# Optimization experiments

Hardware: AMD Instinct MI355X
Metric: run time of the kernel (lower is better)

Reference implementation:

```python
import jax, jax.numpy as jnp
import numpy as np

B, T, H = 16, 512, 1024
L, D = 8192, 256

def setup_inputs() -> dict:
    key = jax.random.key(0)
    k1, k2, k3, k4, k5 = jax.random.split(key, 5)
    X = jax.random.normal(k1, (B, T, H), dtype=jnp.float32)
    attention_mask = jnp.ones((B, T), dtype=jnp.int32)
    queries = jax.random.normal(k2, (L, D), dtype=jnp.float32) * 0.02
    Wk = jax.random.normal(k3, (D, H), dtype=jnp.float32) * (1.0 / np.sqrt(H))
    Wv = jax.random.normal(k4, (D, H), dtype=jnp.float32) * (1.0 / np.sqrt(H))
    out_weight = jax.random.normal(k5, (L, D), dtype=jnp.float32) * 0.02
    out_bias = jnp.zeros((L,), dtype=jnp.float32)
    return {"X": X, "attention_mask": attention_mask, "queries": queries,
            "Wk": Wk, "Wv": Wv, "out_weight": out_weight, "out_bias": out_bias}

def reference(X, attention_mask, queries, Wk, Wv, out_weight, out_bias):
    # K, V: [B, T, D] (nn.Linear with weight [D, H], no bias)
    K = jnp.einsum('bth,dh->btd', X, Wk)
    V = jnp.einsum('bth,dh->btd', X, Wv)
    scale = 1.0 / jnp.sqrt(jnp.asarray(K.shape[-1], dtype=K.dtype))
    # attention logits: [B, L, T]
    attn_logits = jnp.einsum('ld,btd->blt', queries, K) * scale
    neg = jnp.finfo(attn_logits.dtype).min
    attn_logits = jnp.where(attention_mask[:, None, :] == 0, neg, attn_logits)
    attn = jax.nn.softmax(attn_logits, axis=-1)
    # per-label context: [B, L, D]
    ctx = jnp.einsum('blt,btd->bld', attn, V)
    # fused per-label output projection: [B, L]
    logits = jnp.einsum('bld,ld->bl', ctx, out_weight) + out_bias[None, :]
    return logits
```

## Files before the change

kernel.cpp:

```cpp
#include <hip/hip_runtime.h>
#include <hip/hip_bf16.h>


typedef __bf16 bf16x8 __attribute__((ext_vector_type(8)));
typedef float f32x4 __attribute__((ext_vector_type(4)));

__device__ __forceinline__ unsigned short f2bf(float f) {
    unsigned int u = __builtin_bit_cast(unsigned int, f);
    unsigned int lsb = (u >> 16) & 1u;
    u += 0x7fffu + lsb;
    return (unsigned short)(u >> 16);
}

__device__ __forceinline__ void gld_lds16(const void* g, void* l) {
    __builtin_amdgcn_global_load_lds((__attribute__((address_space(1))) void*)g,
                                     (__attribute__((address_space(3))) void*)l,
                                     16, 0, 0);
}

__global__ __launch_bounds__(256) void cvt_all(const float* __restrict__ X,
                                               const float* __restrict__ Q,
                                               const float* __restrict__ Wo,
                                               const float* __restrict__ Wk,
                                               const float* __restrict__ Wv,
                                               unsigned short* __restrict__ dst) {
    int base = blockIdx.x * 1024 + threadIdx.x;
#pragma unroll
    for (int r = 0; r < 4; ++r) {
        int idx = base + r * 256;
        const float* src;
        int off;
        if (idx < 2097152)      { src = X;  off = idx; }
        else if (idx < 2621440) { src = Q;  off = idx - 2097152; }
        else if (idx < 3145728) { src = Wo; off = idx - 2621440; }
        else if (idx < 3211264) { src = Wk; off = idx - 3145728; }
        else                    { src = Wv; off = idx - 3211264; }
        float4 v = ((const float4*)src)[off];
        ushort4 o;
        o.x = f2bf(v.x); o.y = f2bf(v.y); o.z = f2bf(v.z); o.w = f2bf(v.w);
        ((ushort4*)dst)[idx] = o;
    }
}

__global__ __launch_bounds__(256) void kv_gemm(const unsigned short* __restrict__ Xb,
                                               const unsigned short* __restrict__ Wb,
                                               unsigned short* __restrict__ Kb,
                                               unsigned short* __restrict__ Vb) {
    __shared__ unsigned short Xs[128 * 72];
    __shared__ unsigned short Ws[128 * 72];
    const int bid = blockIdx.x;
    const int nt = bid & 3, mt = bid >> 2;
    const int m0 = mt * 128, n0 = nt * 128;
    const int tid = threadIdx.x;
    const int lane = tid & 63, w = tid >> 6;
    const int q = lane >> 4, ln = lane & 15;
    const int wm = (w & 1) * 64, wn = (w >> 1) * 64;

    f32x4 acc[4][4];
#pragma unroll
    for (int mi = 0; mi < 4; ++mi)
#pragma unroll
        for (int ni = 0; ni < 4; ++ni) acc[mi][ni] = f32x4{0.f, 0.f, 0.f, 0.f};

#pragma unroll 1
    for (int h0 = 0; h0 < 1024; h0 += 64) {
#pragma unroll
        for (int i = 0; i < 4; ++i) {
            int c = tid + i * 256;
            int row = c >> 3, off = (c & 7) << 3;
            *(uint4*)(&Xs[row * 72 + off]) = *(const uint4*)(&Xb[(m0 + row) * 1024 + h0 + off]);
            *(uint4*)(&Ws[row * 72 + off]) = *(const uint4*)(&Wb[(n0 + row) * 1024 + h0 + off]);
        }
        __syncthreads();
#pragma unroll
        for (int ks = 0; ks < 64; ks += 32) {
            bf16x8 a[4], b[4];
#pragma unroll
            for (int mi = 0; mi < 4; ++mi)
                a[mi] = *(const bf16x8*)(&Xs[(wm + mi * 16 + ln) * 72 + ks + q * 8]);
#pragma unroll
            for (int ni = 0; ni < 4; ++ni)
                b[ni] = *(const bf16x8*)(&Ws[(wn + ni * 16 + ln) * 72 + ks + q * 8]);
#pragma unroll
            for (int mi = 0; mi < 4; ++mi)
#pragma unroll
                for (int ni = 0; ni < 4; ++ni)
                    acc[mi][ni] = __builtin_amdgcn_mfma_f32_16x16x32_bf16(
                        a[mi], b[ni], acc[mi][ni], 0, 0, 0);
        }
        __syncthreads();
    }
    {
        unsigned short* dst = (n0 < 256) ? Kb : Vb;
        const int d0 = (n0 & 255) + wn;
#pragma unroll
        for (int mi = 0; mi < 4; ++mi)
#pragma unroll
            for (int ni = 0; ni < 4; ++ni) {
                int d = d0 + ni * 16 + ln;
#pragma unroll
                for (int r = 0; r < 4; ++r) {
                    int m = m0 + wm + mi * 16 + q * 4 + r;
                    dst[m * 256 + d] = f2bf(acc[mi][ni][r]);
                }
            }
    }
}

__global__ __launch_bounds__(256, 2) void attn_fused(const unsigned short* __restrict__ Qb,
                                                     const unsigned short* __restrict__ Wob,
                                                     const unsigned short* __restrict__ Kb,
                                                     const unsigned short* __restrict__ Vb,
                                                     const int* __restrict__ mask,
                                                     const float* __restrict__ bias,
                                                     float* __restrict__ out) {
    __shared__ unsigned short Ks[2][8320];
    __shared__ unsigned short Vs[2][8320];
    const int bid = blockIdx.x;
    const int bb = bid >> 6;
    const int l0 = (bid & 63) * 128;
    const int tid = threadIdx.x;
    const int lane = tid & 63, w = tid >> 6;
    const int q = lane >> 4, ln = lane & 15;
    const int laneoff = ((lane >> 3) * 32) + (((lane >> 2) & 1) * 256) + ((lane & 3) * 8);

    bf16x8 aQ[2][8], aW[2][8];
#pragma unroll
    for (int mi = 0; mi < 2; ++mi) {
        const int row = (l0 + w * 32 + mi * 16 + ln) * 256;
#pragma unroll
        for (int kk = 0; kk < 8; ++kk) {
            aQ[mi][kk] = *(const bf16x8*)(&Qb[row + kk * 32 + q * 8]);
            aW[mi][kk] = *(const bf16x8*)(&Wob[row + kk * 32 + q * 8]);
        }
    }

    float num[2][4], den[2][4];
#pragma unroll
    for (int mi = 0; mi < 2; ++mi)
#pragma unroll
        for (int r = 0; r < 4; ++r) { num[mi][r] = 0.f; den[mi][r] = 0.f; }

    auto stage = [&](int c) {
        const int p = c & 1;
        const int rbase = bb * 512 + c * 32;
#pragma unroll
        for (int j = 0; j < 8; ++j) {
            int gid = w * 8 + j;
            int g = gid & 15;
            const unsigned short* srcb = (gid < 16) ? Kb : Vb;
            unsigned short* dstb = (gid < 16) ? &Ks[p][0] : &Vs[p][0];
            gld_lds16(srcb + (((size_t)(rbase + 2 * g)) << 8) + laneoff,
                      dstb + g * 520);
        }
    };
    stage(0);

#pragma unroll 1
    for (int c = 0; c < 16; ++c) {
        __syncthreads();
        if (c < 15) stage(c + 1);
        const int p = c & 1;

        f32x4 Sa[2][2], Pa[2][2];
#pragma unroll
        for (int mi = 0; mi < 2; ++mi)
#pragma unroll
            for (int ni = 0; ni < 2; ++ni) {
                Sa[mi][ni] = f32x4{0.f, 0.f, 0.f, 0.f};
                Pa[mi][ni] = f32x4{0.f, 0.f, 0.f, 0.f};
            }

#pragma unroll
        for (int kk = 0; kk < 8; ++kk) {
            bf16x8 bK[2], bV[2];
#pragma unroll
            for (int ni = 0; ni < 2; ++ni) {
                int rr = ni * 16 + ln;
                int off = (rr >> 1) * 520 + kk * 64 + (rr & 1) * 32 + q * 8;
                bK[ni] = *(const bf16x8*)(&Ks[p][off]);
                bV[ni] = *(const bf16x8*)(&Vs[p][off]);
            }
#pragma unroll
            for (int mi = 0; mi < 2; ++mi)
#pragma unroll
                for (int ni = 0; ni < 2; ++ni) {
                    Sa[mi][ni] = __builtin_amdgcn_mfma_f32_16x16x32_bf16(
                        aQ[mi][kk], bK[ni], Sa[mi][ni], 0, 0, 0);
                    Pa[mi][ni] = __builtin_amdgcn_mfma_f32_16x16x32_bf16(
                        aW[mi][kk], bV[ni], Pa[mi][ni], 0, 0, 0);
                }
        }
#pragma unroll
        for (int ni = 0; ni < 2; ++ni) {
            int t = c * 32 + ni * 16 + ln;
            bool ok = mask[bb * 512 + t] != 0;
#pragma unroll
            for (int mi = 0; mi < 2; ++mi)
#pragma unroll
                for (int r = 0; r < 4; ++r) {
                    float e = ok ? __expf(Sa[mi][ni][r] * 0.0625f) : 0.0f;
                    den[mi][r] += e;
                    num[mi][r] += e * Pa[mi][ni][r];
                }
        }
    }

#pragma unroll
    for (int mi = 0; mi < 2; ++mi)
#pragma unroll
        for (int r = 0; r < 4; ++r) {
            float n_ = num[mi][r], d_ = den[mi][r];
#pragma unroll
            for (int o = 1; o < 16; o <<= 1) {
                n_ += __shfl_xor(n_, o);
                d_ += __shfl_xor(d_, o);
            }
            if (ln == 0) {
                int l = l0 + w * 32 + mi * 16 + q * 4 + r;
                out[bb * 8192 + l] = n_ / d_ + bias[l];
            }
        }
}

extern "C" void kernel_launch(void* const* d_in, const int* in_sizes, int n_in,
                              void* d_out, int out_size, void* d_ws, size_t ws_size,
                              hipStream_t stream) {
    const float* X    = (const float*)d_in[0];
    const int*   mask = (const int*)d_in[1];
    const float* Q    = (const float*)d_in[2];
    const float* Wk   = (const float*)d_in[3];
    const float* Wv   = (const float*)d_in[4];
    const float* Wo   = (const float*)d_in[5];
    const float* bias = (const float*)d_in[6];
    float* out = (float*)d_out;

    unsigned short* Xb   = (unsigned short*)d_ws;
    unsigned short* Qb   = Xb + 8388608ull;
    unsigned short* Wob  = Qb + 2097152ull;
    unsigned short* Wkvb = Wob + 2097152ull;
    unsigned short* Kb   = Wkvb + 524288ull;
    unsigned short* Vb   = Kb + 2097152ull;

    cvt_all<<<dim3(3200), 256, 0, stream>>>(X, Q, Wo, Wk, Wv, Xb);
    kv_gemm<<<dim3(256), 256, 0, stream>>>(Xb, Wkvb, Kb, Vb);
    attn_fused<<<dim3(1024), 256, 0, stream>>>(Qb, Wob, Kb, Vb, mask, bias, out);
}
```

Measured before the change: 201.7 us.

## Fuse fp32-to-bf16 conversion of X and weights into KV GEMM loads

Drops the separate conversion pass for X, Wk and Wv. The KV GEMM now reads fp32 directly and packs to bf16 while filling shared memory, which removes a full write and re-read of the bf16 copy of X. The 1/sqrt(D) scale is folded into Q at conversion time, so the softmax no longer multiplies by it. The attention kernel also stops staging V in LDS and reads the V operands straight from global memory, halving LDS use but adding uncoalesced global loads in the inner loop.

```diff
diff --git a/kernel.cpp b/kernel.cpp
--- a/kernel.cpp
+++ b/kernel.cpp
@@ -12,38 +12,40 @@
     return (unsigned short)(u >> 16);
 }
 
+__device__ __forceinline__ unsigned int pk2(float a, float b) {
+    return (unsigned int)f2bf(a) | ((unsigned int)f2bf(b) << 16);
+}
+
 __device__ __forceinline__ void gld_lds16(const void* g, void* l) {
     __builtin_amdgcn_global_load_lds((__attribute__((address_space(1))) void*)g,
                                      (__attribute__((address_space(3))) void*)l,
                                      16, 0, 0);
 }
 
-__global__ __launch_bounds__(256) void cvt_all(const float* __restrict__ X,
-                                               const float* __restrict__ Q,
-                                               const float* __restrict__ Wo,
+__global__ __launch_bounds__(256) void cvt_qw(const float* __restrict__ Q,
+                                              const float* __restrict__ Wo,
+                                              unsigned short* __restrict__ Qb,
+                                              unsigned short* __restrict__ Wob) {
+    int base = blockIdx.x * 1024 + threadIdx.x;
+#pragma unroll
+    for (int r = 0; r < 4; ++r) {
+        int idx = base + r * 256;
+        bool isQ = idx < 524288;
+        const float* src = isQ ? Q : Wo;
+        unsigned short* dst = isQ ? Qb : Wob;
+        int off = isQ ? idx : idx - 524288;
+        float4 v = ((const float4*)src)[off];
+        float s = isQ ? 0.0625f : 1.0f;
+        uint2 o;
+        o.x = pk2(v.x * s, v.y * s);
+        o.y = pk2(v.z * s, v.w * s);
+        ((uint2*)dst)[off] = o;
+    }
+}
+
+__global__ __launch_bounds__(256) void kv_gemm(const float* __restrict__ Xf,
                                                const float* __restrict__ Wk,
                                                const float* __restrict__ Wv,
-                                               unsigned short* __restrict__ dst) {
-    int base = blockIdx.x * 1024 + threadIdx.x;
-#pragma unroll
-    for (int r = 0; r < 4; ++r) {
-        int idx = base + r * 256;
-        const float* src;
-        int off;
-        if (idx < 2097152)      { src = X;  off = idx; }
-        else if (idx < 2621440) { src = Q;  off = idx - 2097152; }
-        else if (idx < 3145728) { src = Wo; off = idx - 2621440; }
-        else if (idx < 3211264) { src = Wk; off = idx - 3145728; }
-        else                    { src = Wv; off = idx - 3211264; }
-        float4 v = ((const float4*)src)[off];
-        ushort4 o;
-        o.x = f2bf(v.x); o.y = f2bf(v.y); o.z = f2bf(v.z); o.w = f2bf(v.w);
-        ((ushort4*)dst)[idx] = o;
-    }
-}
-
-__global__ __launch_bounds__(256) void kv_gemm(const unsigned short* __restrict__ Xb,
-                                               const unsigned short* __restrict__ Wb,
                                                unsigned short* __restrict__ Kb,
                                                unsigned short* __restrict__ Vb) {
     __shared__ unsigned short Xs[128 * 72];
@@ -55,6 +57,8 @@
     const int lane = tid & 63, w = tid >> 6;
     const int q = lane >> 4, ln = lane & 15;
     const int wm = (w & 1) * 64, wn = (w >> 1) * 64;
+    const float* Wf = (n0 < 256) ? (Wk + (size_t)n0 * 1024)
+                                 : (Wv + (size_t)(n0 - 256) * 1024);
 
     f32x4 acc[4][4];
 #pragma unroll
@@ -68,8 +72,18 @@
         for (int i = 0; i < 4; ++i) {
             int c = tid + i * 256;
             int row = c >> 3, off = (c & 7) << 3;
-            *(uint4*)(&Xs[row * 72 + off]) = *(const uint4*)(&Xb[(m0 + row) * 1024 + h0 + off]);
-            *(uint4*)(&Ws[row * 72 + off]) = *(const uint4*)(&Wb[(n0 + row) * 1024 + h0 + off]);
+            const float* xs = &Xf[(size_t)(m0 + row) * 1024 + h0 + off];
+            float4 x0 = *(const float4*)(xs);
+            float4 x1 = *(const float4*)(xs + 4);
+            uint4 xo = {pk2(x0.x, x0.y), pk2(x0.z, x0.w),
+                        pk2(x1.x, x1.y), pk2(x1.z, x1.w)};
+            *(uint4*)(&Xs[row * 72 + off]) = xo;
+            const float* ws = &Wf[(size_t)row * 1024 + h0 + off];
+            float4 w0 = *(const float4*)(ws);
+            float4 w1 = *(const float4*)(ws + 4);
+            uint4 wo = {pk2(w0.x, w0.y), pk2(w0.z, w0.w),
+                        pk2(w1.x, w1.y), pk2(w1.z, w1.w)};
+            *(uint4*)(&Ws[row * 72 + off]) = wo;
         }
         __syncthreads();
 #pragma unroll
@@ -115,7 +129,6 @@
                                                      const float* __restrict__ bias,
                                                      float* __restrict__ out) {
     __shared__ unsigned short Ks[2][8320];
-    __shared__ unsigned short Vs[2][8320];
     const int bid = blockIdx.x;
     const int bb = bid >> 6;
     const int l0 = (bid & 63) * 128;
@@ -145,16 +158,15 @@
         const int p = c & 1;
         const int rbase = bb * 512 + c * 32;
 #pragma unroll
-        for (int j = 0; j < 8; ++j) {
-            int gid = w * 8 + j;
-            int g = gid & 15;
-            const unsigned short* srcb = (gid < 16) ? Kb : Vb;
-            unsigned short* dstb = (gid < 16) ? &Ks[p][0] : &Vs[p][0];
-            gld_lds16(srcb + (((size_t)(rbase + 2 * g)) << 8) + laneoff,
-                      dstb + g * 520);
+        for (int j = 0; j < 4; ++j) {
+            int g = w * 4 + j;
+            gld_lds16(Kb + (((size_t)(rbase + 2 * g)) << 8) + laneoff,
+                      &Ks[p][g * 520]);
         }
     };
     stage(0);
+
+    const unsigned short* Vbase = Vb + (((size_t)bb) << 17);
 
 #pragma unroll 1
     for (int c = 0; c < 16; ++c) {
@@ -177,9 +189,10 @@
 #pragma unroll
             for (int ni = 0; ni < 2; ++ni) {
                 int rr = ni * 16 + ln;
-                int off = (rr >> 1) * 520 + kk * 64 + (rr & 1) * 32 + q * 8;
-                bK[ni] = *(const bf16x8*)(&Ks[p][off]);
-                bV[ni] = *(const bf16x8*)(&Vs[p][off]);
+                bK[ni] = *(const bf16x8*)(
+                    &Ks[p][(rr >> 1) * 520 + kk * 64 + (rr & 1) * 32 + q * 8]);
+                bV[ni] = *(const bf16x8*)(
+                    &Vbase[((c * 32 + rr) << 8) + kk * 32 + q * 8]);
             }
 #pragma unroll
             for (int mi = 0; mi < 2; ++mi)
@@ -199,7 +212,7 @@
             for (int mi = 0; mi < 2; ++mi)
 #pragma unroll
                 for (int r = 0; r < 4; ++r) {
-                    float e = ok ? __expf(Sa[mi][ni][r] * 0.0625f) : 0.0f;
+                    float e = ok ? __expf(Sa[mi][ni][r]) : 0.0f;
                     den[mi][r] += e;
                     num[mi][r] += e * Pa[mi][ni][r];
                 }
@@ -235,14 +248,12 @@
     const float* bias = (const float*)d_in[6];
     float* out = (float*)d_out;
 
-    unsigned short* Xb   = (unsigned short*)d_ws;
-    unsigned short* Qb   = Xb + 8388608ull;
-    unsigned short* Wob  = Qb + 2097152ull;
-    unsigned short* Wkvb = Wob + 2097152ull;
-    unsigned short* Kb   = Wkvb + 524288ull;
-    unsigned short* Vb   = Kb + 2097152ull;
-
-    cvt_all<<<dim3(3200), 256, 0, stream>>>(X, Q, Wo, Wk, Wv, Xb);
-    kv_gemm<<<dim3(256), 256, 0, stream>>>(Xb, Wkvb, Kb, Vb);
+    unsigned short* Qb  = (unsigned short*)d_ws;
+    unsigned short* Wob = Qb + 2097152ull;
+    unsigned short* Kb  = Wob + 2097152ull;
+    unsigned short* Vb  = Kb + 2097152ull;
+
+    cvt_qw<<<dim3(1024), 256, 0, stream>>>(Q, Wo, Qb, Wob);
+    kv_gemm<<<dim3(256), 256, 0, stream>>>(X, Wk, Wv, Kb, Vb);
     attn_fused<<<dim3(1024), 256, 0, stream>>>(Qb, Wob, Kb, Vb, mask, bias, out);
 }
```

After: 286.8 us. 42.2% more time.
